# Kernel optimization log

Measured on AMD Instinct MI355X. Metric: run time of the kernel, lower is better.

## Reference

```python
import jax, jax.numpy as jnp
import numpy as np

EPS = 1e-5
B, C, H, W, K = 16, 512, 64, 64, 32


def setup_inputs() -> dict:
    key = jax.random.key(0)
    ks = jax.random.split(key, 6)
    std = 1.0 / float(np.sqrt(K * C))
    return {
        "x": jax.random.normal(ks[0], (B, C, H, W), jnp.float32),
        "conv_w": jax.random.normal(ks[1], (C, C), jnp.float32) * (1.0 / np.sqrt(C)),
        "bn2_g": jnp.ones((C,), jnp.float32),
        "bn2_b": jnp.zeros((C,), jnp.float32),
        "bn2_m": jnp.zeros((C,), jnp.float32),
        "bn2_v": jnp.ones((C,), jnp.float32),
        "codewords": jax.random.uniform(ks[2], (K, C), jnp.float32, -std, std),
        "scale": jax.random.uniform(ks[3], (K,), jnp.float32, -1.0, 0.0),
        "bn1_g": jnp.ones((K,), jnp.float32),
        "bn1_b": jnp.zeros((K,), jnp.float32),
        "bn1_m": jnp.zeros((K,), jnp.float32),
        "bn1_v": jnp.ones((K,), jnp.float32),
        "fc_w": jax.random.normal(ks[4], (C, C), jnp.float32) * (1.0 / np.sqrt(C)),
        "fc_b": jnp.zeros((C,), jnp.float32),
    }


def reference(x, conv_w, bn2_g, bn2_b, bn2_m, bn2_v, codewords, scale,
              bn1_g, bn1_b, bn1_m, bn1_v, fc_w, fc_b):
    b, c, h, w = x.shape
    k = codewords.shape[0]
    # encoding_project: 1x1 conv (no bias) + BatchNorm2d (inference) + ReLU
    proj = jnp.einsum('oc,bchw->bohw', conv_w, x)
    s2 = (jax.lax.rsqrt(bn2_v + EPS) * bn2_g)[None, :, None, None]
    proj = jax.nn.relu((proj - bn2_m[None, :, None, None]) * s2 + bn2_b[None, :, None, None])
    # Encoding: scaled-L2 softmax assignment + residual aggregation
    feats = proj.reshape(b, c, h * w).transpose(0, 2, 1)          # (B, N, C)
    x2 = jnp.sum(feats * feats, axis=-1)                          # (B, N)
    c2 = jnp.sum(codewords * codewords, axis=-1)                  # (K,)
    xc = jnp.einsum('bnc,kc->bnk', feats, codewords)              # (B, N, K)
    dist = scale[None, None, :] * (x2[..., None] - 2.0 * xc + c2[None, None, :])
    assign = jax.nn.softmax(dist, axis=2)                         # (B, N, K)
    # sum_n w[b,n,k] * (x[b,n,c] - c[k,c])  without materializing (B,N,K,C)
    encoded = (jnp.einsum('bnk,bnc->bkc', assign, feats)
               - jnp.einsum('bnk,kc->bkc', assign, codewords))    # (B, K, C)
    # BatchNorm1d over num_codes (inference) + ReLU
    s1 = (jax.lax.rsqrt(bn1_v + EPS) * bn1_g)[None, :, None]
    encoded = jax.nn.relu((encoded - bn1_m[None, :, None]) * s1 + bn1_b[None, :, None])
    encoding_feat = jnp.mean(encoded, axis=1)                     # (B, C)
    # fc -> sigmoid gate, residual relu
    gamma = jax.nn.sigmoid(encoding_feat @ fc_w.T + fc_b)         # (B, C)
    output = jax.nn.relu(x + x * gamma[:, :, None, None])
    return (encoding_feat, output)
```

## Files before the change

kernel.cpp:

```cpp
#include <hip/hip_runtime.h>
#include <hip/hip_bf16.h>

#define BB   16
#define CC   512
#define HWN  4096
#define KK   32
#define EPSF 1e-5f

typedef short bf16x8 __attribute__((ext_vector_type(8)));
typedef float f32x4  __attribute__((ext_vector_type(4)));

#define MFMA16 __builtin_amdgcn_mfma_f32_16x16x32_bf16

#define GLD16(g, l) __builtin_amdgcn_global_load_lds(                          \
    (const __attribute__((address_space(1))) void*)(g),                        \
    (__attribute__((address_space(3))) void*)(l), 16, 0, 0)

#define EADDR(o, n) ((o) * 136 + (((((n) >> 3) ^ (((o) >> 3) & 15))) << 3) + ((n) & 7))

static __device__ __forceinline__ unsigned short f2b(float f) {
    unsigned u = __builtin_bit_cast(unsigned, f);
    unsigned r = (u + 0x7FFFu + ((u >> 16) & 1u)) >> 16;
    return (unsigned short)r;
}

__global__ __launch_bounds__(256) void k_prep(const float* __restrict__ W,
                                              const float* __restrict__ cw,
                                              const float* __restrict__ scale,
                                              const float* __restrict__ g1,
                                              const float* __restrict__ b1,
                                              const float* __restrict__ m1,
                                              const float* __restrict__ v1,
                                              unsigned short* __restrict__ Wb,
                                              unsigned short* __restrict__ cwb,
                                              float* __restrict__ sc2,
                                              float* __restrict__ s1,
                                              float* __restrict__ t1) {
    int bid = blockIdx.x, t = threadIdx.x;
    if (bid < 256) {
        int i = (bid * 256 + t) * 4;
        float4 v = *(const float4*)(W + i);
        uint2 p;
        p.x = (unsigned)f2b(v.x) | ((unsigned)f2b(v.y) << 16);
        p.y = (unsigned)f2b(v.z) | ((unsigned)f2b(v.w) << 16);
        *(uint2*)(Wb + i) = p;
    } else if (bid < 272) {
        int i = ((bid - 256) * 256 + t) * 4;
        float4 v = *(const float4*)(cw + i);
        uint2 p;
        p.x = (unsigned)f2b(v.x) | ((unsigned)f2b(v.y) << 16);
        p.y = (unsigned)f2b(v.z) | ((unsigned)f2b(v.w) << 16);
        *(uint2*)(cwb + i) = p;
    } else {
        int k = t >> 3, l8 = t & 7;
        const float* row = cw + k * CC + l8 * 64;
        float s = 0.f;
#pragma unroll
        for (int i = 0; i < 16; i++) {
            float4 c4 = *(const float4*)(row + i * 4);
            s += c4.x * c4.x + c4.y * c4.y + c4.z * c4.z + c4.w * c4.w;
        }
        s += __shfl_xor(s, 1); s += __shfl_xor(s, 2); s += __shfl_xor(s, 4);
        if (l8 == 0) sc2[k] = scale[k] * s;
        if (t < KK) {
            float sv = rsqrtf(v1[t] + EPSF) * g1[t];
            s1[t] = sv;
            t1[t] = b1[t] - m1[t] * sv;
        }
    }
}

#define AADDR(n, c) ((n) * 32 + (((((c) >> 3) ^ (((n) >> 3) & 3)) & 3) << 3) + ((c) & 7))

__global__ __launch_bounds__(256, 4) void k_conv_gemm(const float* __restrict__ x,
                                                      const unsigned short* __restrict__ Wb,
                                                      const float* __restrict__ g2,
                                                      const float* __restrict__ b2,
                                                      const float* __restrict__ m2,
                                                      const float* __restrict__ v2,
                                                      unsigned short* __restrict__ feats,
                                                      unsigned short* __restrict__ featsT,
                                                      float* __restrict__ x2) {
    __shared__ __align__(16) short lds[20480];
    int bid = blockIdx.x;
    bid = (bid & 7) * 256 + (bid >> 3);
    int b   = bid >> 7;
    int rem = bid & 127;
    int m0  = (rem >> 2) * 128;
    int o0  = (rem & 3) * 128;
    int t = threadIdx.x, lane = t & 63, wave = t >> 6;
    int mb = (wave >> 1) * 64, ob = (wave & 1) * 64;
    int col_l = lane & 15, quad = lane >> 4;
    int pc = t >> 4;
    int ch = t & 15;

    f32x4 zero = {0.f, 0.f, 0.f, 0.f};
    f32x4 acc[4][4];
#pragma unroll
    for (int i = 0; i < 4; i++)
#pragma unroll
        for (int j = 0; j < 4; j++) acc[i][j] = zero;

    const float* Xp = x + (size_t)(b * CC) * HWN + m0 + ch * 8;
    const unsigned short* Bbase = Wb + (size_t)o0 * CC;

    float4 a0, a1, a2, a3;

#define CLOAD_A(pp) do {                                                      \
    const float* r0_ = Xp + (size_t)((pp) * 32 + 2 * pc) * HWN;               \
    a0 = *(const float4*)(r0_);       a1 = *(const float4*)(r0_ + 4);         \
    a2 = *(const float4*)(r0_ + HWN); a3 = *(const float4*)(r0_ + HWN + 4);   \
} while (0)

#define CLOAD_B(pp, bb3) do {                                                 \
    int c0_ = (pp) * 32;                                                      \
    _Pragma("unroll")                                                         \
    for (int p2 = 0; p2 < 2; p2++) {                                          \
        int sbase = p2 * 256 + wave * 64;                                     \
        int s = sbase + lane;                                                 \
        GLD16(Bbase + (size_t)(s >> 2) * CC + c0_ + (s & 3) * 8,              \
              (char*)lds + 16384 + (bb3) * 8192 + sbase * 16);                \
    } } while (0)

#define CWRITE_A(ab) do {                                                     \
    unsigned q0, q1, q2, q3, q4, q5, q6, q7;                                  \
    asm("v_cvt_pk_bf16_f32 %0, %1, %2" : "=v"(q0) : "v"(a0.x), "v"(a2.x));    \
    asm("v_cvt_pk_bf16_f32 %0, %1, %2" : "=v"(q1) : "v"(a0.y), "v"(a2.y));    \
    asm("v_cvt_pk_bf16_f32 %0, %1, %2" : "=v"(q2) : "v"(a0.z), "v"(a2.z));    \
    asm("v_cvt_pk_bf16_f32 %0, %1, %2" : "=v"(q3) : "v"(a0.w), "v"(a2.w));    \
    asm("v_cvt_pk_bf16_f32 %0, %1, %2" : "=v"(q4) : "v"(a1.x), "v"(a3.x));    \
    asm("v_cvt_pk_bf16_f32 %0, %1, %2" : "=v"(q5) : "v"(a1.y), "v"(a3.y));    \
    asm("v_cvt_pk_bf16_f32 %0, %1, %2" : "=v"(q6) : "v"(a1.z), "v"(a3.z));    \
    asm("v_cvt_pk_bf16_f32 %0, %1, %2" : "=v"(q7) : "v"(a1.w), "v"(a3.w));    \
    int base_ = (ab) * 4096 + ch * 256 +                                      \
                ((((pc >> 2) ^ (ch & 3)) & 3) << 3) + ((2 * pc) & 7);         \
    *(unsigned*)(&lds[base_ +   0]) = q0;                                     \
    *(unsigned*)(&lds[base_ +  32]) = q1;                                     \
    *(unsigned*)(&lds[base_ +  64]) = q2;                                     \
    *(unsigned*)(&lds[base_ +  96]) = q3;                                     \
    *(unsigned*)(&lds[base_ + 128]) = q4;                                     \
    *(unsigned*)(&lds[base_ + 160]) = q5;                                     \
    *(unsigned*)(&lds[base_ + 192]) = q6;                                     \
    *(unsigned*)(&lds[base_ + 224]) = q7;                                     \
} while (0)

#define CCOMP(ab, bb3) do {                                                   \
    bf16x8 af[4], bfv[4];                                                     \
    _Pragma("unroll")                                                         \
    for (int im = 0; im < 4; im++) {                                          \
        int nl = mb + im * 16 + col_l;                                        \
        af[im] = *(const bf16x8*)(&lds[(ab) * 4096 + AADDR(nl, quad * 8)]);   \
    }                                                                         \
    _Pragma("unroll")                                                         \
    for (int in = 0; in < 4; in++)                                            \
        bfv[in] = *(const bf16x8*)(&lds[8192 + (bb3) * 4096 +                 \
                   (ob + in * 16 + col_l) * 32 + quad * 8]);                  \
    _Pragma("unroll")                                                         \
    for (int im = 0; im < 4; im++)                                            \
        _Pragma("unroll")                                                     \
        for (int in = 0; in < 4; in++)                                        \
            acc[im][in] = MFMA16(af[im], bfv[in], acc[im][in], 0, 0, 0);      \
    } while (0)

    CLOAD_A(0); CLOAD_B(0, 0);
    CWRITE_A(0);
    CLOAD_A(1); CLOAD_B(1, 1);
    asm volatile("s_waitcnt lgkmcnt(0)" ::: "memory");
    asm volatile("s_waitcnt vmcnt(6)" ::: "memory");
    __builtin_amdgcn_s_barrier();
    asm volatile("" ::: "memory");

    int bi = 0;
    for (int p = 0; p < 14; ++p) {
        CCOMP(p & 1, bi);
        CWRITE_A((p + 1) & 1);
        int bi2 = bi >= 1 ? bi - 1 : 2;
        CLOAD_A(p + 2); CLOAD_B(p + 2, bi2);
        asm volatile("s_waitcnt lgkmcnt(0)" ::: "memory");
        asm volatile("s_waitcnt vmcnt(6)" ::: "memory");
        __builtin_amdgcn_s_barrier();
        asm volatile("" ::: "memory");
        bi = bi == 2 ? 0 : bi + 1;
    }
    CCOMP(0, 2);
    CWRITE_A(1);
    asm volatile("s_waitcnt lgkmcnt(0)" ::: "memory");
    asm volatile("s_waitcnt vmcnt(0)" ::: "memory");
    __builtin_amdgcn_s_barrier();
    asm volatile("" ::: "memory");
    CCOMP(1, 0);
    __syncthreads();

    float scv[4], offv[4];
#pragma unroll
    for (int in = 0; in < 4; in++) {
        int o = o0 + ob + in * 16 + col_l;
        float sv = rsqrtf(v2[o] + EPSF) * g2[o];
        scv[in]  = sv;
        offv[in] = b2[o] - m2[o] * sv;
    }
#pragma unroll
    for (int im = 0; im < 4; im++) {
        int n_l = mb + im * 16 + quad * 4;
        float vv[4][4];
#pragma unroll
        for (int in = 0; in < 4; in++)
#pragma unroll
            for (int r = 0; r < 4; r++)
                vv[in][r] = fmaxf(acc[im][in][r] * scv[in] + offv[in], 0.f);
#pragma unroll
        for (int in = 0; in < 4; in++) {
            int o_l = ob + in * 16 + col_l;
            uint2 pk;
            pk.x = (unsigned)f2b(vv[in][0]) | ((unsigned)f2b(vv[in][1]) << 16);
            pk.y = (unsigned)f2b(vv[in][2]) | ((unsigned)f2b(vv[in][3]) << 16);
            *(uint2*)(&lds[EADDR(o_l, n_l)]) = pk;
        }
#pragma unroll
        for (int r = 0; r < 4; r++) {
            float ss = vv[0][r] * vv[0][r] + vv[1][r] * vv[1][r] +
                       vv[2][r] * vv[2][r] + vv[3][r] * vv[3][r];
            ss += __shfl_xor(ss, 1); ss += __shfl_xor(ss, 2);
            ss += __shfl_xor(ss, 4); ss += __shfl_xor(ss, 8);
            if (col_l == 0) atomicAdd(&x2[b * HWN + m0 + n_l + r], ss);
        }
    }
    __syncthreads();

#pragma unroll
    for (int rr = 0; rr < 8; rr++) {
        int o = rr * 16 + (t >> 4);
        int n16 = t & 15;
        uint4 v = *(const uint4*)(&lds[EADDR(o, n16 * 8)]);
        *(uint4*)(featsT + (size_t)(b * CC + o0 + o) * HWN + m0 + n16 * 8) = v;
    }
#pragma unroll
    for (int rr = 0; rr < 8; rr++) {
        int n = rr * 16 + (t >> 4);
        int o16 = t & 15;
        unsigned u[4];
#pragma unroll
        for (int jj = 0; jj < 4; jj++) {
            unsigned short a = lds[EADDR(o16 * 8 + 2 * jj,     n)];
            unsigned short bsh = lds[EADDR(o16 * 8 + 2 * jj + 1, n)];
            u[jj] = (unsigned)a | ((unsigned)bsh << 16);
        }
        uint4 pk; pk.x = u[0]; pk.y = u[1]; pk.z = u[2]; pk.w = u[3];
        *(uint4*)(feats + (size_t)(b * HWN + m0 + n) * CC + o0 + o16 * 8) = pk;
    }
}

__global__ __launch_bounds__(256) void k_assign(const unsigned short* __restrict__ feats,
                                                const unsigned short* __restrict__ cwb,
                                                const float* __restrict__ x2,
                                                const float* __restrict__ scale,
                                                const float* __restrict__ sc2,
                                                unsigned short* __restrict__ assignT,
                                                float* __restrict__ asum) {
    __shared__ __align__(16) short lds2[24832];
    __shared__ float sl[KK], cl[KK];
    int bid = blockIdx.x;
    int b = bid >> 5, n0 = (bid & 31) * 128;
    int t = threadIdx.x, lane = t & 63, wave = t >> 6;
    int col_l = lane & 15, quad = lane >> 4;

#pragma unroll
    for (int p = 0; p < 8; p++) {
        int s = p * 256 + t;
        int row = s >> 6, c8 = (s & 63) * 8;
        *(uint4*)(&lds2[row * 520 + c8]) = *(const uint4*)(cwb + row * 512 + c8);
    }
    if (t < KK) { sl[t] = scale[t]; cl[t] = sc2[t]; }

    f32x4 zero = {0.f, 0.f, 0.f, 0.f};
    f32x4 acc[2][2];
    acc[0][0] = zero; acc[0][1] = zero; acc[1][0] = zero; acc[1][1] = zero;

    const unsigned short* Fbase = feats + (size_t)(b * HWN + n0) * CC;

#define ASTAGE(ci_, bb) do {                                                  \
    int c0_ = (ci_) * 32;                                                     \
    _Pragma("unroll")                                                         \
    for (int p2 = 0; p2 < 2; p2++) {                                          \
        int sbase = p2 * 256 + wave * 64;                                     \
        int s = sbase + lane;                                                 \
        GLD16(Fbase + (size_t)(s >> 2) * CC + c0_ + (s & 3) * 8,              \
              (char*)lds2 + 33280 + (bb) * 8192 + sbase * 16);                \
    } } while (0)

#define ACOMP(ci_, bb) do {                                                   \
    int c0_ = (ci_) * 32;                                                     \
    bf16x8 af0 = *(const bf16x8*)(&lds2[(col_l) * 520 + c0_ + quad * 8]);     \
    bf16x8 af1 = *(const bf16x8*)(&lds2[(16 + col_l) * 520 + c0_ + quad * 8]);\
    _Pragma("unroll")                                                         \
    for (int ct = 0; ct < 2; ct++) {                                          \
        bf16x8 bf = *(const bf16x8*)(&lds2[16640 + (bb) * 4096 +              \
                     (wave * 32 + ct * 16 + col_l) * 32 + quad * 8]);         \
        acc[0][ct] = MFMA16(af0, bf, acc[0][ct], 0, 0, 0);                    \
        acc[1][ct] = MFMA16(af1, bf, acc[1][ct], 0, 0, 0);                    \
    } } while (0)

    ASTAGE(0, 0);
    asm volatile("s_waitcnt lgkmcnt(0)" ::: "memory");
    for (int ci = 0; ci < 15; ci++) {
        ASTAGE(ci + 1, (ci + 1) & 1);
        asm volatile("s_waitcnt vmcnt(2)" ::: "memory");
        __builtin_amdgcn_s_barrier();
        asm volatile("" ::: "memory");
        ACOMP(ci, ci & 1);
        asm volatile("s_waitcnt lgkmcnt(0)" ::: "memory");
        __builtin_amdgcn_s_barrier();
    }
    asm volatile("s_waitcnt vmcnt(0)" ::: "memory");
    __builtin_amdgcn_s_barrier();
    asm volatile("" ::: "memory");
    ACOMP(15, 1);

    float asw[2][4];
#pragma unroll
    for (int mk = 0; mk < 2; mk++)
#pragma unroll
        for (int r = 0; r < 4; r++) asw[mk][r] = 0.f;

#pragma unroll
    for (int ct = 0; ct < 2; ct++) {
        int n = n0 + wave * 32 + ct * 16 + col_l;
        float x2v = x2[b * HWN + n];
        float d[2][4];
        float mmax = -3.4e38f;
#pragma unroll
        for (int mk = 0; mk < 2; mk++)
#pragma unroll
            for (int r = 0; r < 4; r++) {
                int k = mk * 16 + quad * 4 + r;
                d[mk][r] = sl[k] * (x2v - 2.f * acc[mk][ct][r]) + cl[k];
                mmax = fmaxf(mmax, d[mk][r]);
            }
        mmax = fmaxf(mmax, __shfl_xor(mmax, 16));
        mmax = fmaxf(mmax, __shfl_xor(mmax, 32));
        float ssum = 0.f;
#pragma unroll
        for (int mk = 0; mk < 2; mk++)
#pragma unroll
            for (int r = 0; r < 4; r++) {
                d[mk][r] = __expf(d[mk][r] - mmax);
                ssum += d[mk][r];
            }
        ssum += __shfl_xor(ssum, 16);
        ssum += __shfl_xor(ssum, 32);
        float rinv = 1.f / ssum;
#pragma unroll
        for (int mk = 0; mk < 2; mk++)
#pragma unroll
            for (int r = 0; r < 4; r++) {
                int k = mk * 16 + quad * 4 + r;
                float a = d[mk][r] * rinv;
                assignT[(size_t)(b * KK + k) * HWN + n] = f2b(a);
                float p = a;
                p += __shfl_xor(p, 1); p += __shfl_xor(p, 2);
                p += __shfl_xor(p, 4); p += __shfl_xor(p, 8);
                asw[mk][r] += p;
            }
    }
#pragma unroll
    for (int mk = 0; mk < 2; mk++)
#pragma unroll
        for (int r = 0; r < 4; r++)
            if (col_l == 0)
                atomicAdd(&asum[b * KK + mk * 16 + quad * 4 + r], asw[mk][r]);
}

__global__ __launch_bounds__(256) void k_encode(const unsigned short* __restrict__ featsT,
                                                const unsigned short* __restrict__ assignT,
                                                float* __restrict__ enc) {
    __shared__ __align__(16) short lds3[20480];
    int bid = blockIdx.x;
    int b   = bid >> 5;
    int rem = bid & 31;
    int c0  = (rem >> 3) * 128;
    int ns  = rem & 7;
    int t = threadIdx.x, lane = t & 63, wave = t >> 6;
    int col_l = lane & 15, quad = lane >> 4;

    f32x4 zero = {0.f, 0.f, 0.f, 0.f};
    f32x4 acc[2][2];
    acc[0][0] = zero; acc[0][1] = zero; acc[1][0] = zero; acc[1][1] = zero;

    const unsigned short* Abase = featsT + (size_t)(b * CC + c0) * HWN;
    const unsigned short* Bbase = assignT + (size_t)(b * KK) * HWN;

#define ESTAGE(it_, bb) do {                                                  \
    int n0_ = ns * 512 + (it_) * 64;                                          \
    _Pragma("unroll")                                                         \
    for (int pc_ = 0; pc_ < 2; pc_++)                                         \
        _Pragma("unroll")                                                     \
        for (int p2 = 0; p2 < 2; p2++) {                                      \
            int sbase = p2 * 256 + wave * 64;                                 \
            int s = sbase + lane;                                             \
            GLD16(Abase + (size_t)(s >> 2) * HWN + n0_ + pc_ * 32 + (s & 3) * 8, \
                  (char*)lds3 + (bb) * 16384 + pc_ * 8192 + sbase * 16);      \
        }                                                                     \
    {   int s = t;                                                            \
        int pan = s >> 7, row = (s & 127) >> 2, part = (s & 3) * 8;           \
        GLD16(Bbase + (size_t)row * HWN + n0_ + pan * 32 + part,              \
              (char*)lds3 + 32768 + (bb) * 4096 +                             \
              ((wave >> 1) * 2048 + (wave & 1) * 1024) + lane * 16);          \
    } } while (0)

#define ECOMP(bb) do {                                                        \
    _Pragma("unroll")                                                         \
    for (int pc_ = 0; pc_ < 2; pc_++) {                                       \
        bf16x8 a0 = *(const bf16x8*)(&lds3[(bb) * 8192 + pc_ * 4096 + (wave * 32 + col_l) * 32 + quad * 8]); \
        bf16x8 a1 = *(const bf16x8*)(&lds3[(bb) * 8192 + pc_ * 4096 + (wave * 32 + 16 + col_l) * 32 + quad * 8]); \
        bf16x8 b0 = *(const bf16x8*)(&lds3[16384 + (bb) * 2048 + pc_ * 1024 + (col_l) * 32 + quad * 8]); \
        bf16x8 b1 = *(const bf16x8*)(&lds3[16384 + (bb) * 2048 + pc_ * 1024 + (16 + col_l) * 32 + quad * 8]); \
        acc[0][0] = MFMA16(a0, b0, acc[0][0], 0, 0, 0);                       \
        acc[0][1] = MFMA16(a0, b1, acc[0][1], 0, 0, 0);                       \
        acc[1][0] = MFMA16(a1, b0, acc[1][0], 0, 0, 0);                       \
        acc[1][1] = MFMA16(a1, b1, acc[1][1], 0, 0, 0);                       \
    } } while (0)

    ESTAGE(0, 0);
    for (int it = 0; it < 7; it++) {
        ESTAGE(it + 1, (it + 1) & 1);
        asm volatile("s_waitcnt vmcnt(5)" ::: "memory");
        __builtin_amdgcn_s_barrier();
        asm volatile("" ::: "memory");
        ECOMP(it & 1);
        asm volatile("s_waitcnt lgkmcnt(0)" ::: "memory");
        __builtin_amdgcn_s_barrier();
    }
    asm volatile("s_waitcnt vmcnt(0)" ::: "memory");
    __builtin_amdgcn_s_barrier();
    asm volatile("" ::: "memory");
    ECOMP(1);

#pragma unroll
    for (int i2 = 0; i2 < 2; i2++)
#pragma unroll
        for (int ck = 0; ck < 2; ck++)
#pragma unroll
            for (int r = 0; r < 4; r++) {
                int c = c0 + wave * 32 + i2 * 16 + quad * 4 + r;
                int k = ck * 16 + col_l;
                atomicAdd(&enc[(size_t)(b * CC + c) * KK + k], acc[i2][ck][r]);
            }
}

__global__ __launch_bounds__(256) void k_efeat(const float* __restrict__ enc,
                                               const float* __restrict__ asum,
                                               const float* __restrict__ cwf,
                                               const float* __restrict__ s1,
                                               const float* __restrict__ t1,
                                               float* __restrict__ efeat) {
    __shared__ float asl[KK], s1l[KK], t1l[KK];
    int b = blockIdx.x, t = threadIdx.x;
    if (t < KK) { asl[t] = asum[b * KK + t]; s1l[t] = s1[t]; t1l[t] = t1[t]; }
    __syncthreads();
#pragma unroll
    for (int cc = 0; cc < 2; cc++) {
        int c = cc * 256 + t;
        const float* er = enc + (size_t)(b * CC + c) * KK;
        float s = 0.f;
#pragma unroll
        for (int k = 0; k < KK; k++) {
            float v = (er[k] - asl[k] * cwf[k * CC + c]) * s1l[k] + t1l[k];
            s += fmaxf(v, 0.f);
        }
        efeat[b * CC + c] = s * (1.f / 32.f);
    }
}

__global__ __launch_bounds__(256) void k_fc(const float* __restrict__ efeat,
                                            const float* __restrict__ fcw,
                                            const float* __restrict__ fcb,
                                            float* __restrict__ gamma) {
    __shared__ float ef[CC];
    int bid = blockIdx.x;
    int b  = bid >> 1;
    int o0 = (bid & 1) * 256;
    int t = threadIdx.x;
    if (t < 128) *(float4*)(&ef[t * 4]) = *(const float4*)(efeat + b * CC + t * 4);
    __syncthreads();
    int o = o0 + t;
    float a = fcb[o];
    const float* wrow = fcw + (size_t)o * CC;
#pragma unroll 4
    for (int c4 = 0; c4 < 128; c4++) {
        float4 w = *(const float4*)(wrow + c4 * 4);
        float4 e = *(const float4*)(&ef[c4 * 4]);
        a += w.x * e.x + w.y * e.y + w.z * e.z + w.w * e.w;
    }
    gamma[b * CC + o] = 1.f / (1.f + __expf(-a));
}

__global__ __launch_bounds__(256) void k_gate(const float* __restrict__ x,
                                              const float* __restrict__ gamma,
                                              float* __restrict__ out) {
    int bid = blockIdx.x;
    float g = 1.f + gamma[bid];
    const float* xr = x + ((size_t)bid << 12);
    float* orow = out + ((size_t)bid << 12);
    int t4 = threadIdx.x * 4;
#pragma unroll
    for (int u = 0; u < 4; u++) {
        float4 v = *(const float4*)(xr + u * 1024 + t4);
        v.x = fmaxf(v.x * g, 0.f);
        v.y = fmaxf(v.y * g, 0.f);
        v.z = fmaxf(v.z * g, 0.f);
        v.w = fmaxf(v.w * g, 0.f);
        *(float4*)(orow + u * 1024 + t4) = v;
    }
}

extern "C" void kernel_launch(void* const* d_in, const int* in_sizes, int n_in,
                              void* d_out, int out_size, void* d_ws, size_t ws_size,
                              hipStream_t stream) {
    const float* x      = (const float*)d_in[0];
    const float* conv_w = (const float*)d_in[1];
    const float* bn2_g  = (const float*)d_in[2];
    const float* bn2_b  = (const float*)d_in[3];
    const float* bn2_m  = (const float*)d_in[4];
    const float* bn2_v  = (const float*)d_in[5];
    const float* cw     = (const float*)d_in[6];
    const float* scale  = (const float*)d_in[7];
    const float* bn1_g  = (const float*)d_in[8];
    const float* bn1_b  = (const float*)d_in[9];
    const float* bn1_m  = (const float*)d_in[10];
    const float* bn1_v  = (const float*)d_in[11];
    const float* fc_w   = (const float*)d_in[12];
    const float* fc_b   = (const float*)d_in[13];

    float* outf = (float*)d_out;
    char* ws = (char*)d_ws;

    unsigned short* feats   = (unsigned short*)(ws);
    unsigned short* assignT = (unsigned short*)(ws + 67108864);
    unsigned short* Wb      = (unsigned short*)(ws + 71303168);
    unsigned short* cwb     = (unsigned short*)(ws + 71827456);
    float*          x2      = (float*)(ws + 71860224);
    float*          asum    = (float*)(ws + 72122368);
    float*          enc     = (float*)(ws + 72124416);
    float*          sc2     = (float*)(ws + 73172992);
    float*          s1      = (float*)(ws + 73173248);
    float*          t1      = (float*)(ws + 73173504);
    float*          gamma   = (float*)(ws + 73173760);

    unsigned short* featsT = (unsigned short*)((char*)d_out + 67141632);

    hipMemsetAsync(x2, 0, 262144 + 2048 + 1048576, stream);

    k_prep<<<273, 256, 0, stream>>>(conv_w, cw, scale, bn1_g, bn1_b, bn1_m, bn1_v,
                                    Wb, cwb, sc2, s1, t1);
    k_conv_gemm<<<2048, 256, 0, stream>>>(x, Wb, bn2_g, bn2_b, bn2_m, bn2_v,
                                          feats, featsT, x2);
    k_assign<<<512, 256, 0, stream>>>(feats, cwb, x2, scale, sc2, assignT, asum);
    k_encode<<<512, 256, 0, stream>>>(featsT, assignT, enc);
    k_efeat<<<16, 256, 0, stream>>>(enc, asum, cw, s1, t1, outf);
    k_fc<<<32, 256, 0, stream>>>(outf, fc_w, fc_b, gamma);
    k_gate<<<8192, 256, 0, stream>>>(x, gamma, outf + 8192);
}
```

Before: 420.5 us.

## Deepen conv GEMM A-prefetch to two stages and fuse efeat with fc

New measurement: 522.0 us. 1.24x slower.

```diff
diff --git a/kernel.cpp b/kernel.cpp
--- a/kernel.cpp
+++ b/kernel.cpp
@@ -104,12 +104,13 @@
     const float* Xp = x + (size_t)(b * CC) * HWN + m0 + ch * 8;
     const unsigned short* Bbase = Wb + (size_t)o0 * CC;
 
-    float4 a0, a1, a2, a3;
-
-#define CLOAD_A(pp) do {                                                      \
+    float4 A00, A01, A02, A03;
+    float4 A10, A11, A12, A13;
+
+#define CLOAD_AX(pp, R0, R1, R2, R3) do {                                     \
     const float* r0_ = Xp + (size_t)((pp) * 32 + 2 * pc) * HWN;               \
-    a0 = *(const float4*)(r0_);       a1 = *(const float4*)(r0_ + 4);         \
-    a2 = *(const float4*)(r0_ + HWN); a3 = *(const float4*)(r0_ + HWN + 4);   \
+    R0 = *(const float4*)(r0_);       R1 = *(const float4*)(r0_ + 4);         \
+    R2 = *(const float4*)(r0_ + HWN); R3 = *(const float4*)(r0_ + HWN + 4);   \
 } while (0)
 
 #define CLOAD_B(pp, bb3) do {                                                 \
@@ -122,26 +123,26 @@
               (char*)lds + 16384 + (bb3) * 8192 + sbase * 16);                \
     } } while (0)
 
-#define CWRITE_A(ab) do {                                                     \
-    unsigned q0, q1, q2, q3, q4, q5, q6, q7;                                  \
-    asm("v_cvt_pk_bf16_f32 %0, %1, %2" : "=v"(q0) : "v"(a0.x), "v"(a2.x));    \
-    asm("v_cvt_pk_bf16_f32 %0, %1, %2" : "=v"(q1) : "v"(a0.y), "v"(a2.y));    \
-    asm("v_cvt_pk_bf16_f32 %0, %1, %2" : "=v"(q2) : "v"(a0.z), "v"(a2.z));    \
-    asm("v_cvt_pk_bf16_f32 %0, %1, %2" : "=v"(q3) : "v"(a0.w), "v"(a2.w));    \
-    asm("v_cvt_pk_bf16_f32 %0, %1, %2" : "=v"(q4) : "v"(a1.x), "v"(a3.x));    \
-    asm("v_cvt_pk_bf16_f32 %0, %1, %2" : "=v"(q5) : "v"(a1.y), "v"(a3.y));    \
-    asm("v_cvt_pk_bf16_f32 %0, %1, %2" : "=v"(q6) : "v"(a1.z), "v"(a3.z));    \
-    asm("v_cvt_pk_bf16_f32 %0, %1, %2" : "=v"(q7) : "v"(a1.w), "v"(a3.w));    \
+#define CWRITE_AX(ab, R0, R1, R2, R3) do {                                    \
+    unsigned u0, u1, u2, u3, u4, u5, u6, u7;                                  \
+    asm("v_cvt_pk_bf16_f32 %0, %1, %2" : "=v"(u0) : "v"(R0.x), "v"(R2.x));    \
+    asm("v_cvt_pk_bf16_f32 %0, %1, %2" : "=v"(u1) : "v"(R0.y), "v"(R2.y));    \
+    asm("v_cvt_pk_bf16_f32 %0, %1, %2" : "=v"(u2) : "v"(R0.z), "v"(R2.z));    \
+    asm("v_cvt_pk_bf16_f32 %0, %1, %2" : "=v"(u3) : "v"(R0.w), "v"(R2.w));    \
+    asm("v_cvt_pk_bf16_f32 %0, %1, %2" : "=v"(u4) : "v"(R1.x), "v"(R3.x));    \
+    asm("v_cvt_pk_bf16_f32 %0, %1, %2" : "=v"(u5) : "v"(R1.y), "v"(R3.y));    \
+    asm("v_cvt_pk_bf16_f32 %0, %1, %2" : "=v"(u6) : "v"(R1.z), "v"(R3.z));    \
+    asm("v_cvt_pk_bf16_f32 %0, %1, %2" : "=v"(u7) : "v"(R1.w), "v"(R3.w));    \
     int base_ = (ab) * 4096 + ch * 256 +                                      \
                 ((((pc >> 2) ^ (ch & 3)) & 3) << 3) + ((2 * pc) & 7);         \
-    *(unsigned*)(&lds[base_ +   0]) = q0;                                     \
-    *(unsigned*)(&lds[base_ +  32]) = q1;                                     \
-    *(unsigned*)(&lds[base_ +  64]) = q2;                                     \
-    *(unsigned*)(&lds[base_ +  96]) = q3;                                     \
-    *(unsigned*)(&lds[base_ + 128]) = q4;                                     \
-    *(unsigned*)(&lds[base_ + 160]) = q5;                                     \
-    *(unsigned*)(&lds[base_ + 192]) = q6;                                     \
-    *(unsigned*)(&lds[base_ + 224]) = q7;                                     \
+    *(unsigned*)(&lds[base_ +   0]) = u0;                                     \
+    *(unsigned*)(&lds[base_ +  32]) = u1;                                     \
+    *(unsigned*)(&lds[base_ +  64]) = u2;                                     \
+    *(unsigned*)(&lds[base_ +  96]) = u3;                                     \
+    *(unsigned*)(&lds[base_ + 128]) = u4;                                     \
+    *(unsigned*)(&lds[base_ + 160]) = u5;                                     \
+    *(unsigned*)(&lds[base_ + 192]) = u6;                                     \
+    *(unsigned*)(&lds[base_ + 224]) = u7;                                     \
 } while (0)
 
 #define CCOMP(ab, bb3) do {                                                   \
@@ -162,28 +163,51 @@
             acc[im][in] = MFMA16(af[im], bfv[in], acc[im][in], 0, 0, 0);      \
     } while (0)
 
-    CLOAD_A(0); CLOAD_B(0, 0);
-    CWRITE_A(0);
-    CLOAD_A(1); CLOAD_B(1, 1);
+#define STEP(p, AB, BB, NB, R0, R1, R2, R3) do {                              \
+    CWRITE_AX((AB) ^ 1, R0, R1, R2, R3);                                      \
+    CCOMP(AB, BB);                                                            \
+    CLOAD_AX((p) + 3, R0, R1, R2, R3);                                        \
+    CLOAD_B((p) + 2, NB);                                                     \
+    asm volatile("s_waitcnt lgkmcnt(0)" ::: "memory");                        \
+    asm volatile("s_waitcnt vmcnt(6)" ::: "memory");                          \
+    __builtin_amdgcn_s_barrier();                                             \
+    asm volatile("" ::: "memory");                                            \
+} while (0)
+
+    CLOAD_AX(0, A00, A01, A02, A03); CLOAD_B(0, 0);
+    CLOAD_AX(1, A10, A11, A12, A13); CLOAD_B(1, 1);
+    CWRITE_AX(0, A00, A01, A02, A03);
+    CLOAD_AX(2, A00, A01, A02, A03);
+    asm volatile("s_waitcnt lgkmcnt(0)" ::: "memory");
+    asm volatile("s_waitcnt vmcnt(10)" ::: "memory");
+    __builtin_amdgcn_s_barrier();
+    asm volatile("" ::: "memory");
+
+    for (int p = 0; p < 12; p += 6) {
+        STEP(p + 0, 0, 0, 2, A10, A11, A12, A13);
+        STEP(p + 1, 1, 1, 0, A00, A01, A02, A03);
+        STEP(p + 2, 0, 2, 1, A10, A11, A12, A13);
+        STEP(p + 3, 1, 0, 2, A00, A01, A02, A03);
+        STEP(p + 4, 0, 1, 0, A10, A11, A12, A13);
+        STEP(p + 5, 1, 2, 1, A00, A01, A02, A03);
+    }
+    CWRITE_AX(1, A10, A11, A12, A13);
+    CCOMP(0, 0);
+    CLOAD_AX(15, A10, A11, A12, A13);
+    CLOAD_B(14, 2);
     asm volatile("s_waitcnt lgkmcnt(0)" ::: "memory");
     asm volatile("s_waitcnt vmcnt(6)" ::: "memory");
     __builtin_amdgcn_s_barrier();
     asm volatile("" ::: "memory");
-
-    int bi = 0;
-    for (int p = 0; p < 14; ++p) {
-        CCOMP(p & 1, bi);
-        CWRITE_A((p + 1) & 1);
-        int bi2 = bi >= 1 ? bi - 1 : 2;
-        CLOAD_A(p + 2); CLOAD_B(p + 2, bi2);
-        asm volatile("s_waitcnt lgkmcnt(0)" ::: "memory");
-        asm volatile("s_waitcnt vmcnt(6)" ::: "memory");
-        __builtin_amdgcn_s_barrier();
-        asm volatile("" ::: "memory");
-        bi = bi == 2 ? 0 : bi + 1;
-    }
+    CWRITE_AX(0, A00, A01, A02, A03);
+    CCOMP(1, 1);
+    CLOAD_B(15, 0);
+    asm volatile("s_waitcnt lgkmcnt(0)" ::: "memory");
+    asm volatile("s_waitcnt vmcnt(2)" ::: "memory");
+    __builtin_amdgcn_s_barrier();
+    asm volatile("" ::: "memory");
+    CWRITE_AX(1, A10, A11, A12, A13);
     CCOMP(0, 2);
-    CWRITE_A(1);
     asm volatile("s_waitcnt lgkmcnt(0)" ::: "memory");
     asm volatile("s_waitcnt vmcnt(0)" ::: "memory");
     __builtin_amdgcn_s_barrier();
@@ -447,13 +471,17 @@
             }
 }
 
-__global__ __launch_bounds__(256) void k_efeat(const float* __restrict__ enc,
-                                               const float* __restrict__ asum,
-                                               const float* __restrict__ cwf,
-                                               const float* __restrict__ s1,
-                                               const float* __restrict__ t1,
-                                               float* __restrict__ efeat) {
+__global__ __launch_bounds__(256) void k_efeat_fc(const float* __restrict__ enc,
+                                                  const float* __restrict__ asum,
+                                                  const float* __restrict__ cwf,
+                                                  const float* __restrict__ s1,
+                                                  const float* __restrict__ t1,
+                                                  const float* __restrict__ fcw,
+                                                  const float* __restrict__ fcb,
+                                                  float* __restrict__ efeat,
+                                                  float* __restrict__ gamma) {
     __shared__ float asl[KK], s1l[KK], t1l[KK];
+    __shared__ float ef[CC];
     int b = blockIdx.x, t = threadIdx.x;
     if (t < KK) { asl[t] = asum[b * KK + t]; s1l[t] = s1[t]; t1l[t] = t1[t]; }
     __syncthreads();
@@ -467,31 +495,24 @@
             float v = (er[k] - asl[k] * cwf[k * CC + c]) * s1l[k] + t1l[k];
             s += fmaxf(v, 0.f);
         }
-        efeat[b * CC + c] = s * (1.f / 32.f);
-    }
-}
-
-__global__ __launch_bounds__(256) void k_fc(const float* __restrict__ efeat,
-                                            const float* __restrict__ fcw,
-                                            const float* __restrict__ fcb,
-                                            float* __restrict__ gamma) {
-    __shared__ float ef[CC];
-    int bid = blockIdx.x;
-    int b  = bid >> 1;
-    int o0 = (bid & 1) * 256;
-    int t = threadIdx.x;
-    if (t < 128) *(float4*)(&ef[t * 4]) = *(const float4*)(efeat + b * CC + t * 4);
+        s *= (1.f / 32.f);
+        ef[c] = s;
+        efeat[b * CC + c] = s;
+    }
     __syncthreads();
-    int o = o0 + t;
-    float a = fcb[o];
-    const float* wrow = fcw + (size_t)o * CC;
+#pragma unroll
+    for (int oo = 0; oo < 2; oo++) {
+        int o = oo * 256 + t;
+        float a = fcb[o];
+        const float* wrow = fcw + (size_t)o * CC;
 #pragma unroll 4
-    for (int c4 = 0; c4 < 128; c4++) {
-        float4 w = *(const float4*)(wrow + c4 * 4);
-        float4 e = *(const float4*)(&ef[c4 * 4]);
-        a += w.x * e.x + w.y * e.y + w.z * e.z + w.w * e.w;
-    }
-    gamma[b * CC + o] = 1.f / (1.f + __expf(-a));
+        for (int c4 = 0; c4 < 128; c4++) {
+            float4 w = *(const float4*)(wrow + c4 * 4);
+            float4 e = *(const float4*)(&ef[c4 * 4]);
+            a += w.x * e.x + w.y * e.y + w.z * e.z + w.w * e.w;
+        }
+        gamma[b * CC + o] = 1.f / (1.f + __expf(-a));
+    }
 }
 
 __global__ __launch_bounds__(256) void k_gate(const float* __restrict__ x,
@@ -556,7 +577,6 @@
                                           feats, featsT, x2);
     k_assign<<<512, 256, 0, stream>>>(feats, cwb, x2, scale, sc2, assignT, asum);
     k_encode<<<512, 256, 0, stream>>>(featsT, assignT, enc);
-    k_efeat<<<16, 256, 0, stream>>>(enc, asum, cw, s1, t1, outf);
-    k_fc<<<32, 256, 0, stream>>>(outf, fc_w, fc_b, gamma);
+    k_efeat_fc<<<16, 256, 0, stream>>>(enc, asum, cw, s1, t1, fc_w, fc_b, outf, gamma);
     k_gate<<<8192, 256, 0, stream>>>(x, gamma, outf + 8192);
 }
```
